# Kernel optimization log

Measured on AMD Instinct MI355X. Metric: run time of the kernel, lower is better.

## Reference

```python
import jax, jax.numpy as jnp
import numpy as np

B, N, D, H = 4, 1024, 512, 16
DH = D // H
FACTOR = 0.5 / np.sqrt(DH).astype(np.float32)


def setup_inputs() -> dict:
    key = jax.random.key(0)
    ks = jax.random.split(key, 16)
    w = lambda k, shape: (jax.random.normal(k, shape, dtype=jnp.float32) * 0.02)
    return {
        "H": jax.random.normal(ks[0], (B, N, D), dtype=jnp.float32),
        "V": jax.random.normal(ks[1], (B, N, 3, D), dtype=jnp.float32),
        "D_batch": jax.random.normal(ks[2], (B, N, N), dtype=jnp.float32),
        "rbf_feat": jax.random.normal(ks[3], (1, B, H, N, N), dtype=jnp.float32),
        "H_mask": jax.random.randint(ks[4], (B, N), 0, 2).astype(jnp.int32),
        "Wq": w(ks[5], (4 * D, D)), "bq": w(ks[6], (4 * D,)),
        "Wk": w(ks[7], (4 * D, D)), "bk": w(ks[8], (4 * D,)),
        "Wv": w(ks[9], (D, D)), "bv": w(ks[10], (D,)),
        "Wvv": w(ks[11], (D, D)),
        "Wo": w(ks[12], (D, D)), "bo": w(ks[13], (D,)),
        "Wvo": w(ks[14], (D, D)),
    }


def reference(H, V, D_batch, rbf_feat, H_mask, Wq, bq, Wk, bk, Wv, bv, Wvv, Wo, bo, Wvo):
    b, n, d = H.shape
    h = rbf_feat.shape[2]
    dh = d // h
    # projections
    H_q = (H @ Wq.T + bq).reshape(b, n, h, 4 * dh)
    H_k = (H @ Wk.T + bk).reshape(b, n, h, 4 * dh)
    H_v = (H @ Wv.T + bv).reshape(b, n, h, dh)
    # vector values: [b,n,3,d] -> [b,n,3,h,dh] -> [b,n,h,3,dh] -> [b,n,h,3*dh]
    V_v = jnp.einsum('bncd,ed->bnce', V, Wvv)
    V_v = jnp.swapaxes(V_v.reshape(b, n, 3, h, dh), -2, -3).reshape(b, n, h, 3 * dh)
    V_attn = jnp.concatenate([H_v, V_v], axis=-1)  # [b,n,h,4*dh]
    # additive bias + key mask
    bias = rbf_feat[0] + D_batch[:, None]            # [b,h,n,n]
    mask = (H_mask[:, None, None, :] != 0)           # [b,1,1,n]
    bias = jnp.where(mask, bias, -jnp.inf)
    scores = jnp.einsum('bnhd,bmhd->bhnm', H_q, H_k) * jnp.float32(FACTOR) + bias
    attn = jax.nn.softmax(scores, axis=-1)
    res = jnp.einsum('bhnm,bmhd->bnhd', attn, V_attn)  # [b,n,h,4*dh]
    H_res = res[..., :dh].reshape(b, n, d)
    V_res = jnp.swapaxes(res[..., dh:].reshape(b, n, h, 3, dh), -2, -3).reshape(b, n, 3, d)
    H_o = H_res @ Wo.T + bo
    V_o = jnp.einsum('bncd,ed->bnce', V_res, Wvo)
    return (H_o, V_o)
```

## Files before the change

### kernel.cpp

```cpp
#include <hip/hip_runtime.h>
#include <cmath>

#define FACTOR 0.08838834764831845f

typedef short s16x8 __attribute__((ext_vector_type(8)));
typedef float f32x4 __attribute__((ext_vector_type(4)));
typedef float f32x16 __attribute__((ext_vector_type(16)));
typedef unsigned int u32;

#define KEEP_LOADS() do { asm volatile("" ::: "memory"); __builtin_amdgcn_sched_barrier(0); } while (0)

__device__ __forceinline__ unsigned short f2bf(float x) {
  unsigned int u = __float_as_uint(x);
  u += 0x7FFFu + ((u >> 16) & 1u);
  return (unsigned short)(u >> 16);
}

__device__ __forceinline__ s16x8 pack8(float4 a, float4 b) {
  s16x8 r;
  r[0] = (short)f2bf(a.x); r[1] = (short)f2bf(a.y);
  r[2] = (short)f2bf(a.z); r[3] = (short)f2bf(a.w);
  r[4] = (short)f2bf(b.x); r[5] = (short)f2bf(b.y);
  r[6] = (short)f2bf(b.z); r[7] = (short)f2bf(b.w);
  return r;
}

__device__ __forceinline__ void gload_lds16(const void* g, void* l) {
  __builtin_amdgcn_global_load_lds(
      (const __attribute__((address_space(1))) u32*)g,
      (__attribute__((address_space(3))) u32*)l, 16, 0, 0);
}

__device__ __forceinline__ void gemm_body(
    const float* __restrict__ A, const float* __restrict__ B,
    const float* __restrict__ bias, void* __restrict__ C,
    int N, int K, int mode, int gx, int gy,
    unsigned short* As, unsigned short* Bs)
{
  const int tid = threadIdx.x;
  const int w = tid >> 6, lane = tid & 63;
  const int l16 = lane & 15, lg = lane >> 4;
  const int wm = w >> 1, wn = w & 1;
  const int m0 = gx * 128;
  const int n0 = gy * 128;

  const int sr = tid >> 3;
  const int sc = (tid & 7) * 8;

  float4 ar[4][2], br[4][2];

  auto issue = [&](int k0) {
#pragma unroll
    for (int i = 0; i < 4; ++i) {
      const int rr = i * 32 + sr;
      const float* ap = A + (size_t)(m0 + rr) * K + k0 + sc;
      ar[i][0] = *(const float4*)ap;
      ar[i][1] = *(const float4*)(ap + 4);
      const float* bp;
      if (mode == 5) {
        const int t = n0 + rr;
        const int q3 = t >> 10, n = t & 1023;
        const int bb = q3 / 3, cd = q3 - 3 * bb;
        bp = B + (((size_t)(bb * 1024 + n)) * 3 + cd) * 512 + k0 + sc;
      } else {
        bp = B + (size_t)(n0 + rr) * K + k0 + sc;
      }
      br[i][0] = *(const float4*)bp;
      br[i][1] = *(const float4*)(bp + 4);
    }
  };

  f32x4 acc[4][4];
#pragma unroll
  for (int mt = 0; mt < 4; ++mt)
#pragma unroll
    for (int nt = 0; nt < 4; ++nt)
#pragma unroll
      for (int r = 0; r < 4; ++r) acc[mt][nt][r] = 0.f;

  issue(0);

#pragma unroll 1
  for (int k0 = 0; k0 < K; k0 += 64) {
    __builtin_amdgcn_s_barrier();
#pragma unroll
    for (int i = 0; i < 4; ++i) {
      const int rr = i * 32 + sr;
      *(s16x8*)&As[rr * 72 + sc] = pack8(ar[i][0], ar[i][1]);
      *(s16x8*)&Bs[rr * 72 + sc] = pack8(br[i][0], br[i][1]);
    }
    asm volatile("s_waitcnt lgkmcnt(0)" ::: "memory");
    __builtin_amdgcn_s_barrier();
    if (k0 + 64 < K) issue(k0 + 64);
    KEEP_LOADS();

#pragma unroll
    for (int ks = 0; ks < 2; ++ks) {
      s16x8 af[4], bf[4];
#pragma unroll
      for (int mt = 0; mt < 4; ++mt)
        af[mt] = *(const s16x8*)&As[(wm * 64 + mt * 16 + l16) * 72 + ks * 32 + lg * 8];
#pragma unroll
      for (int nt = 0; nt < 4; ++nt)
        bf[nt] = *(const s16x8*)&Bs[(wn * 64 + nt * 16 + l16) * 72 + ks * 32 + lg * 8];
#pragma unroll
      for (int mt = 0; mt < 4; ++mt)
#pragma unroll
        for (int nt = 0; nt < 4; ++nt)
          acc[mt][nt] = __builtin_amdgcn_mfma_f32_16x16x32_bf16(af[mt], bf[nt], acc[mt][nt], 0, 0, 0);
    }
  }

  const int rbase = m0 + wm * 64;
  const int cbase = n0 + wn * 64;

  if (mode == 0 || mode == 3) {
#pragma unroll
    for (int nt = 0; nt < 4; ++nt) {
      const int c = cbase + nt * 16 + l16;
      const float bb = bias ? bias[c] : 0.f;
#pragma unroll
      for (int mt = 0; mt < 4; ++mt) {
#pragma unroll
        for (int r = 0; r < 4; ++r) {
          const int row = rbase + mt * 16 + lg * 4 + r;
          const float v = acc[mt][nt][r] + bb;
          if (mode == 0) ((float*)C)[(size_t)row * N + c] = v;
          else           ((unsigned short*)C)[(size_t)row * N + c] = f2bf(v);
        }
      }
    }
  } else {
    unsigned short* Cb = (unsigned short*)C;
#pragma unroll
    for (int mt = 0; mt < 4; ++mt) {
#pragma unroll
      for (int r = 0; r < 4; ++r) {
        const int ch = rbase + mt * 16 + lg * 4 + r;
        const float bb = bias ? bias[ch] : 0.f;
        const int h = ch >> 5, dq = ch & 31;
#pragma unroll
        for (int nt = 0; nt < 4; ++nt) {
          const int t = cbase + nt * 16 + l16;
          size_t off;
          if (mode == 4) {
            const int b = t >> 10, n = t & 1023;
            off = (((size_t)(b * 16 + h)) * 128 + dq) * 1024 + n;
          } else {
            const int q3 = t >> 10, n = t & 1023;
            const int b = q3 / 3, cd = q3 - 3 * b;
            off = (((size_t)(b * 16 + h)) * 128 + 32 + cd * 32 + dq) * 1024 + n;
          }
          Cb[off] = f2bf(acc[mt][nt][r] + bb);
        }
      }
    }
  }
}

__global__ __launch_bounds__(256) void gemm_proj(
    const float* __restrict__ Hp, const float* __restrict__ Vp,
    const float* __restrict__ Wq, const float* __restrict__ bq,
    const float* __restrict__ Wk, const float* __restrict__ bk,
    const float* __restrict__ Wv, const float* __restrict__ bv,
    const float* __restrict__ Wvv,
    unsigned short* __restrict__ Qb, unsigned short* __restrict__ Kb,
    unsigned short* __restrict__ Vt)
{
  __shared__ unsigned short As[128 * 72];
  __shared__ unsigned short Bs[128 * 72];

  int blk = blockIdx.x;
  if (blk < 512) {
    gemm_body(Hp, Wq, bq, Qb, 2048, 512, 3, blk & 31, blk >> 5, As, Bs);
  } else if (blk < 1024) {
    blk -= 512;
    gemm_body(Hp, Wk, bk, Kb, 2048, 512, 3, blk & 31, blk >> 5, As, Bs);
  } else if (blk < 1152) {
    blk -= 1024;
    gemm_body(Wv, Hp, bv, Vt, 4096, 512, 4, blk & 3, blk >> 2, As, Bs);
  } else {
    blk -= 1152;
    gemm_body(Wvv, Vp, nullptr, Vt, 12288, 512, 5, blk & 3, blk >> 2, As, Bs);
  }
}

__global__ __launch_bounds__(256) void gemm_out(
    const float* __restrict__ Hres, const float* __restrict__ Vres,
    const float* __restrict__ Wo, const float* __restrict__ bo,
    const float* __restrict__ Wvo, float* __restrict__ out)
{
  __shared__ unsigned short As[128 * 72];
  __shared__ unsigned short Bs[128 * 72];

  int blk = blockIdx.x;
  if (blk < 128) {
    gemm_body(Hres, Wo, bo, out, 512, 512, 0, blk & 31, blk >> 5, As, Bs);
  } else {
    blk -= 128;
    gemm_body(Vres, Wvo, nullptr, out + 2097152, 512, 512, 0, blk % 96, blk / 96, As, Bs);
  }
}

__global__ __launch_bounds__(256, 2) void attn_mfma(
    const unsigned short* __restrict__ Qg, const unsigned short* __restrict__ Kg,
    const unsigned short* __restrict__ Vtg, const float* __restrict__ rbf,
    const float* __restrict__ Dm, const int* __restrict__ msk,
    float* __restrict__ Hres, float* __restrict__ Vres)
{
  __shared__ unsigned short KsL[2][4096];
  __shared__ unsigned short VtL[2][4096];
  __shared__ int   MsL[1024];
  __shared__ float RbL[128 * 32];
  __shared__ float DbL[128 * 32];
  __shared__ float SsL[4][32 * 18];

  const int tid  = threadIdx.x;
  const int w    = tid >> 6;
  const int lane = tid & 63;
  const int l32  = lane & 31;
  const int hi   = lane >> 5;

  const int bh = blockIdx.y;
  const int b  = bh >> 4;
  const int h  = bh & 15;
  const int q0 = blockIdx.x * 128 + w * 32;

  s16x8 qf[8];
  {
    const unsigned short* qp = Qg + ((size_t)(b * 1024 + q0 + l32)) * 2048 + h * 128 + hi * 8;
#pragma unroll
    for (int ks = 0; ks < 8; ++ks) qf[ks] = *(const s16x8*)(qp + ks * 16);
  }

  f32x16 acc[4];
  float m_run = -INFINITY, l_run = 0.f;
#pragma unroll
  for (int dt = 0; dt < 4; ++dt)
#pragma unroll
    for (int r = 0; r < 16; ++r) acc[dt][r] = 0.f;

  auto issue_kv = [&](int t, int bf) {
    const int m0 = t * 32;
#pragma unroll
    for (int jj = 0; jj < 2; ++jj) {
      const int i = w * 2 + jj;
      gload_lds16(Kg + ((size_t)(b * 1024 + m0 + l32)) * 2048 + h * 128 + (2 * i + hi) * 8,
                  &KsL[bf][i * 512]);
      gload_lds16(Vtg + ((size_t)(bh * 128 + (i >> 1) * 32 + l32)) * 1024 + m0 + ((i & 1) * 2 + hi) * 8,
                  &VtL[bf][i * 512]);
    }
  };

  auto issue_bias = [&](int t) {
    const int m0 = t * 32;
#pragma unroll
    for (int i = 0; i < 4; ++i) {
      const int qq = q0 + i * 8 + (lane >> 3);
      const int ch = (lane & 7) * 4;
      gload_lds16(rbf + ((size_t)bh * 1024 + qq) * 1024 + m0 + ch, &RbL[w * 1024 + i * 256]);
      gload_lds16(Dm  + ((size_t)b  * 1024 + qq) * 1024 + m0 + ch, &DbL[w * 1024 + i * 256]);
    }
  };

  gload_lds16(msk + b * 1024 + w * 256 + lane * 4, &MsL[w * 256]);
  issue_kv(0, 0);
  issue_bias(0);

#pragma unroll 1
  for (int t = 0; t < 32; ++t) {
    const int bf = t & 1;
    const int m0 = t * 32;

    asm volatile("s_waitcnt vmcnt(0)" ::: "memory");
    __builtin_amdgcn_s_barrier();

    if (t < 31) issue_kv(t + 1, bf ^ 1);
    __builtin_amdgcn_sched_barrier(0);

    f32x16 sf;
#pragma unroll
    for (int r = 0; r < 16; ++r) sf[r] = 0.f;
    __builtin_amdgcn_s_setprio(1);
#pragma unroll
    for (int ks = 0; ks < 8; ++ks) {
      const s16x8 kf = *(const s16x8*)&KsL[bf][(ks * 2 + hi) * 256 + l32 * 8];
      sf = __builtin_amdgcn_mfma_f32_32x32x16_bf16(qf[ks], kf, sf, 0, 0, 0);
    }
    __builtin_amdgcn_s_setprio(0);

    const bool on = MsL[m0 + l32] != 0;
    float sv[16];
#pragma unroll
    for (int r = 0; r < 16; ++r) {
      const int ql = (r & 3) + 8 * (r >> 2) + 4 * hi;
      const float bb = RbL[w * 1024 + ql * 32 + l32] + DbL[w * 1024 + ql * 32 + l32];
      sv[r] = on ? fmaf(sf[r], FACTOR, bb) : -INFINITY;
    }
    asm volatile("s_waitcnt lgkmcnt(0)" ::: "memory");
    __builtin_amdgcn_sched_barrier(0);
    if (t < 31) issue_bias(t + 1);
    __builtin_amdgcn_sched_barrier(0);

    float s[16];
    if (l32 < 16) {
#pragma unroll
      for (int r = 0; r < 16; ++r) {
        const int ql = (r & 3) + 8 * (r >> 2) + 4 * hi;
        SsL[w][ql * 18 + l32] = sv[r];
      }
    }
    asm volatile("s_waitcnt lgkmcnt(0)" ::: "memory");
    __builtin_amdgcn_sched_barrier(0);
    if (hi == 0) {
#pragma unroll
      for (int j = 0; j < 16; ++j) s[j] = SsL[w][l32 * 18 + j];
    }
    __builtin_amdgcn_sched_barrier(0);
    if (l32 >= 16) {
#pragma unroll
      for (int r = 0; r < 16; ++r) {
        const int ql = (r & 3) + 8 * (r >> 2) + 4 * hi;
        SsL[w][ql * 18 + (l32 - 16)] = sv[r];
      }
    }
    asm volatile("s_waitcnt lgkmcnt(0)" ::: "memory");
    __builtin_amdgcn_sched_barrier(0);
    if (hi == 1) {
#pragma unroll
      for (int j = 0; j < 16; ++j) s[j] = SsL[w][l32 * 18 + j];
    }
    __builtin_amdgcn_sched_barrier(0);

    float mx = s[0];
#pragma unroll
    for (int j = 1; j < 16; ++j) mx = fmaxf(mx, s[j]);
    const float tmax = fmaxf(mx, __shfl_xor(mx, 32));

    const bool ok = (tmax <= m_run + 8.f);
    if (!__all(ok ? 1 : 0)) {
      const float mn = fmaxf(m_run, tmax);
      const float sc = (mn == m_run) ? 1.f : __expf(m_run - mn);
      m_run = mn;
      l_run *= sc;
#pragma unroll
      for (int dt = 0; dt < 4; ++dt)
#pragma unroll
        for (int r = 0; r < 16; ++r) acc[dt][r] *= sc;
    }

    float psv[16];
    float rs = 0.f;
#pragma unroll
    for (int j = 0; j < 16; ++j) {
      psv[j] = (s[j] == -INFINITY) ? 0.f : __expf(s[j] - m_run);
      rs += psv[j];
    }
    l_run += rs;

    {
      u32* Pw = (u32*)&SsL[w][0];
#pragma unroll
      for (int j = 0; j < 8; ++j) {
        const u32 word = (u32)f2bf(psv[2 * j]) | ((u32)f2bf(psv[2 * j + 1]) << 16);
        Pw[l32 * 18 + hi * 8 + j] = word;
      }
    }
    asm volatile("s_waitcnt lgkmcnt(0)" ::: "memory");
    __builtin_amdgcn_sched_barrier(0);

    const unsigned short* Pr = (const unsigned short*)&SsL[w][0];
    const s16x8 pf0 = *(const s16x8*)&Pr[l32 * 36 + hi * 8];
    const s16x8 pf1 = *(const s16x8*)&Pr[l32 * 36 + 16 + hi * 8];

    __builtin_amdgcn_s_setprio(1);
#pragma unroll
    for (int dt = 0; dt < 4; ++dt) {
      const s16x8 vf0 = *(const s16x8*)&VtL[bf][dt * 1024 + hi * 256 + l32 * 8];
      const s16x8 vf1 = *(const s16x8*)&VtL[bf][dt * 1024 + (2 + hi) * 256 + l32 * 8];
      acc[dt] = __builtin_amdgcn_mfma_f32_32x32x16_bf16(vf0, pf0, acc[dt], 0, 0, 0);
      acc[dt] = __builtin_amdgcn_mfma_f32_32x32x16_bf16(vf1, pf1, acc[dt], 0, 0, 0);
    }
    __builtin_amdgcn_s_setprio(0);
  }

  const float lt = l_run + __shfl_xor(l_run, 32);
  const float inv = (lt > 0.f) ? 1.f / lt : 0.f;

  const int q = q0 + l32;
#pragma unroll
  for (int dt = 0; dt < 4; ++dt) {
#pragma unroll
    for (int r = 0; r < 16; ++r) {
      const int dloc = (r & 3) + 8 * (r >> 2) + 4 * hi;
      const float o = acc[dt][r] * inv;
      if (dt == 0) {
        Hres[((size_t)(b * 1024 + q)) * 512 + h * 32 + dloc] = o;
      } else {
        Vres[(((size_t)(b * 1024 + q)) * 3 + (dt - 1)) * 512 + h * 32 + dloc] = o;
      }
    }
  }
}

extern "C" void kernel_launch(void* const* d_in, const int* in_sizes, int n_in,
                              void* d_out, int out_size, void* d_ws, size_t ws_size,
                              hipStream_t stream)
{
  const float* Hp  = (const float*)d_in[0];
  const float* Vp  = (const float*)d_in[1];
  const float* Db  = (const float*)d_in[2];
  const float* rbf = (const float*)d_in[3];
  const int*   Hm  = (const int*)d_in[4];
  const float* Wq  = (const float*)d_in[5];
  const float* bq  = (const float*)d_in[6];
  const float* Wk  = (const float*)d_in[7];
  const float* bk  = (const float*)d_in[8];
  const float* Wv  = (const float*)d_in[9];
  const float* bv  = (const float*)d_in[10];
  const float* Wvv = (const float*)d_in[11];
  const float* Wo  = (const float*)d_in[12];
  const float* bo  = (const float*)d_in[13];
  const float* Wvo = (const float*)d_in[14];
  float* out = (float*)d_out;

  if (ws_size < (size_t)83886080) return;
  unsigned short* Qb = (unsigned short*)d_ws;
  unsigned short* Kb = Qb + 8388608;
  unsigned short* Vt = Kb + 8388608;
  float* Hres = (float*)(Vt + 8388608);
  float* Vres = Hres + 2097152;

  const dim3 blk(256);

  gemm_proj<<<dim3(1536), blk, 0, stream>>>(Hp, Vp, Wq, bq, Wk, bk, Wv, bv, Wvv,
                                            Qb, Kb, Vt);

  attn_mfma<<<dim3(8, 64), blk, 0, stream>>>(Qb, Kb, Vt, rbf, Db, Hm, Hres, Vres);

  gemm_out<<<dim3(512), blk, 0, stream>>>(Hres, Vres, Wo, bo, Wvo, out);
}
```

Before: 256.7 us.

## Transpose QK MFMA output to skip LDS score transpose, swizzle bias tiles

```diff
diff --git a/kernel.cpp b/kernel.cpp
--- a/kernel.cpp
+++ b/kernel.cpp
@@ -213,7 +213,6 @@
   __shared__ int   MsL[1024];
   __shared__ float RbL[128 * 32];
   __shared__ float DbL[128 * 32];
-  __shared__ float SsL[4][32 * 18];
 
   const int tid  = threadIdx.x;
   const int w    = tid >> 6;
@@ -257,7 +256,7 @@
 #pragma unroll
     for (int i = 0; i < 4; ++i) {
       const int qq = q0 + i * 8 + (lane >> 3);
-      const int ch = (lane & 7) * 4;
+      const int ch = ((((lane & 7) + (lane >> 3)) & 7)) * 4;
       gload_lds16(rbf + ((size_t)bh * 1024 + qq) * 1024 + m0 + ch, &RbL[w * 1024 + i * 256]);
       gload_lds16(Dm  + ((size_t)b  * 1024 + qq) * 1024 + m0 + ch, &DbL[w * 1024 + i * 256]);
     }
@@ -285,56 +284,35 @@
 #pragma unroll
     for (int ks = 0; ks < 8; ++ks) {
       const s16x8 kf = *(const s16x8*)&KsL[bf][(ks * 2 + hi) * 256 + l32 * 8];
-      sf = __builtin_amdgcn_mfma_f32_32x32x16_bf16(qf[ks], kf, sf, 0, 0, 0);
+      sf = __builtin_amdgcn_mfma_f32_32x32x16_bf16(kf, qf[ks], sf, 0, 0, 0);
     }
     __builtin_amdgcn_s_setprio(0);
 
-    const bool on = MsL[m0 + l32] != 0;
+    f32x4 rbq[4], dbq[4];
+    int4  mq[4];
+#pragma unroll
+    for (int g = 0; g < 4; ++g) {
+      const int slot = ((g * 2 + hi) - (l32 & 7)) & 7;
+      rbq[g] = *(const f32x4*)&RbL[w * 1024 + l32 * 32 + slot * 4];
+      dbq[g] = *(const f32x4*)&DbL[w * 1024 + l32 * 32 + slot * 4];
+      mq[g]  = *(const int4*)&MsL[m0 + g * 8 + 4 * hi];
+    }
     float sv[16];
 #pragma unroll
     for (int r = 0; r < 16; ++r) {
-      const int ql = (r & 3) + 8 * (r >> 2) + 4 * hi;
-      const float bb = RbL[w * 1024 + ql * 32 + l32] + DbL[w * 1024 + ql * 32 + l32];
-      sv[r] = on ? fmaf(sf[r], FACTOR, bb) : -INFINITY;
+      const int g = r >> 2, e = r & 3;
+      const int mk = (e == 0) ? mq[g].x : (e == 1) ? mq[g].y : (e == 2) ? mq[g].z : mq[g].w;
+      const float bb = rbq[g][e] + dbq[g][e];
+      sv[r] = mk ? fmaf(sf[r], FACTOR, bb) : -INFINITY;
     }
     asm volatile("s_waitcnt lgkmcnt(0)" ::: "memory");
     __builtin_amdgcn_sched_barrier(0);
     if (t < 31) issue_bias(t + 1);
     __builtin_amdgcn_sched_barrier(0);
 
-    float s[16];
-    if (l32 < 16) {
-#pragma unroll
-      for (int r = 0; r < 16; ++r) {
-        const int ql = (r & 3) + 8 * (r >> 2) + 4 * hi;
-        SsL[w][ql * 18 + l32] = sv[r];
-      }
-    }
-    asm volatile("s_waitcnt lgkmcnt(0)" ::: "memory");
-    __builtin_amdgcn_sched_barrier(0);
-    if (hi == 0) {
-#pragma unroll
-      for (int j = 0; j < 16; ++j) s[j] = SsL[w][l32 * 18 + j];
-    }
-    __builtin_amdgcn_sched_barrier(0);
-    if (l32 >= 16) {
-#pragma unroll
-      for (int r = 0; r < 16; ++r) {
-        const int ql = (r & 3) + 8 * (r >> 2) + 4 * hi;
-        SsL[w][ql * 18 + (l32 - 16)] = sv[r];
-      }
-    }
-    asm volatile("s_waitcnt lgkmcnt(0)" ::: "memory");
-    __builtin_amdgcn_sched_barrier(0);
-    if (hi == 1) {
-#pragma unroll
-      for (int j = 0; j < 16; ++j) s[j] = SsL[w][l32 * 18 + j];
-    }
-    __builtin_amdgcn_sched_barrier(0);
-
-    float mx = s[0];
-#pragma unroll
-    for (int j = 1; j < 16; ++j) mx = fmaxf(mx, s[j]);
+    float mx = sv[0];
+#pragma unroll
+    for (int r = 1; r < 16; ++r) mx = fmaxf(mx, sv[r]);
     const float tmax = fmaxf(mx, __shfl_xor(mx, 32));
 
     const bool ok = (tmax <= m_run + 8.f);
@@ -352,34 +330,37 @@
     float psv[16];
     float rs = 0.f;
 #pragma unroll
-    for (int j = 0; j < 16; ++j) {
-      psv[j] = (s[j] == -INFINITY) ? 0.f : __expf(s[j] - m_run);
-      rs += psv[j];
+    for (int r = 0; r < 16; ++r) {
+      psv[r] = (sv[r] == -INFINITY) ? 0.f : __expf(sv[r] - m_run);
+      rs += psv[r];
     }
     l_run += rs;
 
-    {
-      u32* Pw = (u32*)&SsL[w][0];
-#pragma unroll
-      for (int j = 0; j < 8; ++j) {
-        const u32 word = (u32)f2bf(psv[2 * j]) | ((u32)f2bf(psv[2 * j + 1]) << 16);
-        Pw[l32 * 18 + hi * 8 + j] = word;
+    u32 pk[4][2], sw[4][2];
+#pragma unroll
+    for (int g = 0; g < 4; ++g)
+#pragma unroll
+      for (int j = 0; j < 2; ++j) {
+        pk[g][j] = (u32)f2bf(psv[4 * g + 2 * j]) | ((u32)f2bf(psv[4 * g + 2 * j + 1]) << 16);
+        sw[g][j] = (u32)__shfl_xor((int)pk[g][j], 32);
       }
-    }
-    asm volatile("s_waitcnt lgkmcnt(0)" ::: "memory");
-    __builtin_amdgcn_sched_barrier(0);
-
-    const unsigned short* Pr = (const unsigned short*)&SsL[w][0];
-    const s16x8 pf0 = *(const s16x8*)&Pr[l32 * 36 + hi * 8];
-    const s16x8 pf1 = *(const s16x8*)&Pr[l32 * 36 + 16 + hi * 8];
+    union { u32 u[4]; s16x8 v; } P0, P1;
+    P0.u[0] = hi ? sw[1][0] : pk[0][0];
+    P0.u[1] = hi ? sw[1][1] : pk[0][1];
+    P0.u[2] = hi ? pk[1][0] : sw[0][0];
+    P0.u[3] = hi ? pk[1][1] : sw[0][1];
+    P1.u[0] = hi ? sw[3][0] : pk[2][0];
+    P1.u[1] = hi ? sw[3][1] : pk[2][1];
+    P1.u[2] = hi ? pk[3][0] : sw[2][0];
+    P1.u[3] = hi ? pk[3][1] : sw[2][1];
 
     __builtin_amdgcn_s_setprio(1);
 #pragma unroll
     for (int dt = 0; dt < 4; ++dt) {
       const s16x8 vf0 = *(const s16x8*)&VtL[bf][dt * 1024 + hi * 256 + l32 * 8];
       const s16x8 vf1 = *(const s16x8*)&VtL[bf][dt * 1024 + (2 + hi) * 256 + l32 * 8];
-      acc[dt] = __builtin_amdgcn_mfma_f32_32x32x16_bf16(vf0, pf0, acc[dt], 0, 0, 0);
-      acc[dt] = __builtin_amdgcn_mfma_f32_32x32x16_bf16(vf1, pf1, acc[dt], 0, 0, 0);
+      acc[dt] = __builtin_amdgcn_mfma_f32_32x32x16_bf16(vf0, P0.v, acc[dt], 0, 0, 0);
+      acc[dt] = __builtin_amdgcn_mfma_f32_32x32x16_bf16(vf1, P1.v, acc[dt], 0, 0, 0);
     }
     __builtin_amdgcn_s_setprio(0);
   }
```

After: 235.7 us (median of 3 runs). -8.2%, faster.
